# Performance work log

Measured on AMD Instinct MI355X. Metric: run time of the kernel, lower is better.

The kernel has to match this reference:

```python
import jax, jax.numpy as jnp
import numpy as np

B, N_REG, D_IN = 32, 116, 256
N_NODES = B * N_REG            # 3712
E_PER_G = N_REG * 10           # avg degree 10
E = B * E_PER_G                # 37120
HEADS = 8
HID = [256, 128, 64]
D_OUT = 256
LN_EPS = 1e-5


def _layer_norm(x, scale, bias):
    mu = x.mean(-1, keepdims=True)
    var = ((x - mu) ** 2).mean(-1, keepdims=True)
    return (x - mu) * jax.lax.rsqrt(var + LN_EPS) * scale + bias


def _gat_layer(x, W, b, a_src, a_dst, src, dst, concat):
    """PyG-style GATConv (shared lin, self-loops, leaky_relu 0.2) + ELU + LayerNorm."""
    N = x.shape[0]
    H, C = a_src.shape
    h = (x @ W).reshape(N, H, C)                      # (N, H, C)
    sl = jnp.arange(N, dtype=src.dtype)               # self-loops (PyG default)
    s = jnp.concatenate([src, sl])
    d = jnp.concatenate([dst, sl])
    al = (h * a_src).sum(-1)                          # (N, H)
    ar = (h * a_dst).sum(-1)                          # (N, H)
    e = jax.nn.leaky_relu(al[s] + ar[d], 0.2)         # (E', H)
    m = jax.ops.segment_max(e, d, num_segments=N)
    ex = jnp.exp(e - m[d])
    den = jax.ops.segment_sum(ex, d, num_segments=N)
    alpha = ex / den[d]                               # segment softmax over incoming edges
    out = jax.ops.segment_sum(h[s] * alpha[..., None], d, num_segments=N)  # (N, H, C)
    out = out.reshape(N, H * C) if concat else out.mean(1)
    return out + b


def setup_inputs() -> dict:
    key = jax.random.key(0)
    ks = list(jax.random.split(key, 32))
    node_features = jax.random.normal(ks[0], (N_NODES, D_IN), dtype=jnp.float32)
    # edges: random within each graph (disconnected batched graph)
    off = (jnp.arange(B, dtype=jnp.int32) * N_REG)[:, None]
    src = (jax.random.randint(ks[1], (B, E_PER_G), 0, N_REG, dtype=jnp.int32) + off).reshape(-1)
    dst = (jax.random.randint(ks[2], (B, E_PER_G), 0, N_REG, dtype=jnp.int32) + off).reshape(-1)
    batch = jnp.repeat(jnp.arange(B, dtype=jnp.int32), N_REG)

    def lin(k, fin, fout):
        s = 1.0 / np.sqrt(fin)
        return jax.random.uniform(k, (fin, fout), jnp.float32, -s, s)

    dims_in = [D_IN, HID[0] * HEADS, HID[1] * HEADS]
    p = {}
    ki = 3
    for i, (fin, c) in enumerate(zip(dims_in, HID)):
        concat = i < len(HID) - 1
        wdim = c * HEADS
        p[f"w{i}"] = lin(ks[ki], fin, wdim); ki += 1
        p[f"b{i}"] = jnp.zeros((wdim if concat else c,), jnp.float32)
        p[f"as{i}"] = jax.random.normal(ks[ki], (HEADS, c), jnp.float32) * 0.1; ki += 1
        p[f"ad{i}"] = jax.random.normal(ks[ki], (HEADS, c), jnp.float32) * 0.1; ki += 1
        ldim = wdim if concat else c
        p[f"ls{i}"] = jnp.ones((ldim,), jnp.float32)
        p[f"lb{i}"] = jnp.zeros((ldim,), jnp.float32)
    p["wp"] = lin(ks[ki], HID[-1], D_OUT); ki += 1
    p["bp"] = jnp.zeros((D_OUT,), jnp.float32)
    p["lsp"] = jnp.ones((D_OUT,), jnp.float32)
    p["lbp"] = jnp.zeros((D_OUT,), jnp.float32)
    p["wq"] = lin(ks[ki], D_OUT, 1); ki += 1
    p["bq"] = jnp.zeros((1,), jnp.float32)
    return dict(node_features=node_features, src=src, dst=dst, batch=batch, **p)


def reference(node_features, src, dst, batch,
              w0, b0, as0, ad0, ls0, lb0,
              w1, b1, as1, ad1, ls1, lb1,
              w2, b2, as2, ad2, ls2, lb2,
              wp, bp, lsp, lbp, wq, bq):
    x = node_features
    x = _layer_norm(jax.nn.elu(_gat_layer(x, w0, b0, as0, ad0, src, dst, True)), ls0, lb0)
    x = _layer_norm(jax.nn.elu(_gat_layer(x, w1, b1, as1, ad1, src, dst, True)), ls1, lb1)
    x = _layer_norm(jax.nn.elu(_gat_layer(x, w2, b2, as2, ad2, src, dst, False)), ls2, lb2)
    node_out = jax.nn.gelu(_layer_norm(x @ wp + bp, lsp, lbp), approximate=False)  # (N, 256)
    pool_w = jax.nn.softmax(node_out @ wq + bq, axis=0)                            # (N, 1) global softmax
    num = jax.ops.segment_sum(node_out * pool_w, batch, num_segments=B)            # (B, 256)
    den = jnp.maximum(jax.ops.segment_sum(pool_w, batch, num_segments=B), 1e-8)    # (B, 1)
    graph_features = num / den
    return graph_features, node_out
```

## Files before the change

### kernel.cpp

```cpp
#include <hip/hip_runtime.h>
#include <hip/hip_bf16.h>
#include <math.h>

typedef __hip_bfloat16 bf16;
typedef short short8 __attribute__((ext_vector_type(8)));
typedef float f32x4 __attribute__((ext_vector_type(4)));

__device__ __forceinline__ float b2f(const bf16 v) { return __bfloat162float(v); }
__device__ __forceinline__ bf16 f2b(const float v) { return __float2bfloat16(v); }

__device__ __forceinline__ float bits2f(short s) {
  unsigned u = ((unsigned)(unsigned short)s) << 16;
  float f;
  __builtin_memcpy(&f, &u, 4);
  return f;
}
__device__ __forceinline__ short f2bits(float f) {
  bf16 b = f2b(f);
  short s;
  __builtin_memcpy(&s, &b, 2);
  return s;
}

__device__ __forceinline__ float ldsel(const void* p, size_t i, int f32) {
  return f32 ? ((const float*)p)[i] : b2f(((const bf16*)p)[i]);
}
__device__ __forceinline__ void stsel(void* p, size_t i, float v, int f32) {
  if (f32) ((float*)p)[i] = v; else ((bf16*)p)[i] = f2b(v);
}

#define NN 3712
#define NE 37120
#define NG 32
#define NREG 116
#define MAXDEG 48

__global__ __launch_bounds__(256) void k_detect(const void* nf, const void* w0, int* flags) {
  __shared__ int bad[2];
  if (threadIdx.x < 2) bad[threadIdx.x] = 0;
  __syncthreads();
  const bf16* a = (const bf16*)nf;
  const bf16* b = (const bf16*)w0;
  int l0 = 0, l1 = 0;
  for (int i = threadIdx.x; i < 4096; i += 256) {
    float x = b2f(a[i]); if (!(fabsf(x) < 1e4f)) l0++;
    float y = b2f(b[i]); if (!(fabsf(y) < 1e4f)) l1++;
  }
  if (l0) atomicAdd(&bad[0], l0);
  if (l1) atomicAdd(&bad[1], l1);
  __syncthreads();
  if (threadIdx.x == 0) { flags[0] = bad[0] > 0; flags[1] = bad[1] > 0; }
}

__global__ __launch_bounds__(256) void k_zero(int* __restrict__ p, int n) {
  int i = blockIdx.x * 256 + threadIdx.x;
  if (i < n) p[i] = 0;
}

__global__ __launch_bounds__(256) void k_scatter(const int* __restrict__ src, const int* __restrict__ dst,
                                                 int* __restrict__ cnt, int* __restrict__ bucket, int E) {
  int e = blockIdx.x * 256 + threadIdx.x;
  if (e < E) {
    int d = dst[e], s = src[e];
    if ((unsigned)d < NN && (unsigned)s < NN) {
      int p = atomicAdd(&cnt[d], 1);
      if (p < MAXDEG) bucket[d * MAXDEG + p] = s;
    }
  }
}

__global__ __launch_bounds__(256) void k_tobf16(const void* __restrict__ in, bf16* __restrict__ out,
                                                int n, const int* __restrict__ flags, int fidx) {
  int f = flags[fidx];
  int i = blockIdx.x * 256 + threadIdx.x;
  if (i < n) out[i] = f2b(ldsel(in, i, f));
}

__global__ __launch_bounds__(256) void k_transpose(const void* __restrict__ W, bf16* __restrict__ Wt,
                                                   int K, int N, const int* __restrict__ flags) {
  int f = flags[1];
  __shared__ float tile[32][33];
  int tx = threadIdx.x & 31, ty = threadIdx.x >> 5;
  int k0 = blockIdx.x * 32, n0 = blockIdx.y * 32;
#pragma unroll
  for (int i = 0; i < 4; ++i)
    tile[ty + i * 8][tx] = ldsel(W, (size_t)(k0 + ty + i * 8) * N + n0 + tx, f);
  __syncthreads();
#pragma unroll
  for (int i = 0; i < 4; ++i)
    Wt[(size_t)(n0 + ty + i * 8) * K + k0 + tx] = f2b(tile[tx][ty + i * 8]);
}

__global__ __launch_bounds__(256) void k_gemm_mfma(const bf16* __restrict__ A, const bf16* __restrict__ Bt,
                                                   bf16* __restrict__ C, int M, int N, int K) {
  __shared__ short As[64 * 72];
  __shared__ short Bs[64 * 72];
  int tid = threadIdx.x;
  int wave = tid >> 6, lane = tid & 63;
  int wr = wave >> 1, wc = wave & 1;
  int quad = lane >> 4, ml = lane & 15;

  int nbx = N >> 6;
  int total = gridDim.x;
  int id = blockIdx.x;
  int tile = ((total & 7) == 0) ? ((id & 7) * (total >> 3) + (id >> 3)) : id;
  int n0 = (tile % nbx) << 6;
  int m0 = (tile / nbx) << 6;

  f32x4 acc[2][2];
#pragma unroll
  for (int rt = 0; rt < 2; ++rt)
#pragma unroll
    for (int ct = 0; ct < 2; ++ct)
#pragma unroll
      for (int r = 0; r < 4; ++r) acc[rt][ct][r] = 0.f;

  for (int k0 = 0; k0 < K; k0 += 64) {
    __syncthreads();
#pragma unroll
    for (int i = 0; i < 2; ++i) {
      int c = tid + (i << 8);
      int row = c >> 3, kg = (c & 7) << 3;
      *(uint4*)&As[row * 72 + kg] = *(const uint4*)&A[(size_t)(m0 + row) * K + k0 + kg];
      *(uint4*)&Bs[row * 72 + kg] = *(const uint4*)&Bt[(size_t)(n0 + row) * K + k0 + kg];
    }
    __syncthreads();
    short8 af[2][2], bfr[2][2];
#pragma unroll
    for (int rt = 0; rt < 2; ++rt)
#pragma unroll
      for (int kk = 0; kk < 2; ++kk)
        af[rt][kk] = *(const short8*)&As[(wr * 32 + rt * 16 + ml) * 72 + kk * 32 + quad * 8];
#pragma unroll
    for (int ct = 0; ct < 2; ++ct)
#pragma unroll
      for (int kk = 0; kk < 2; ++kk)
        bfr[ct][kk] = *(const short8*)&Bs[(wc * 32 + ct * 16 + ml) * 72 + kk * 32 + quad * 8];
#pragma unroll
    for (int rt = 0; rt < 2; ++rt)
#pragma unroll
      for (int ct = 0; ct < 2; ++ct)
#pragma unroll
        for (int kk = 0; kk < 2; ++kk)
          acc[rt][ct] = __builtin_amdgcn_mfma_f32_16x16x32_bf16(af[rt][kk], bfr[ct][kk], acc[rt][ct], 0, 0, 0);
  }
#pragma unroll
  for (int rt = 0; rt < 2; ++rt)
#pragma unroll
    for (int ct = 0; ct < 2; ++ct)
#pragma unroll
      for (int r = 0; r < 4; ++r) {
        int grow = m0 + wr * 32 + rt * 16 + quad * 4 + r;
        int gcol = n0 + wc * 32 + ct * 16 + ml;
        C[(size_t)grow * N + gcol] = f2b(acc[rt][ct][r]);
      }
}

__global__ void k_attn(const bf16* __restrict__ H, const void* __restrict__ a_s,
                       const void* __restrict__ a_d, float* __restrict__ al,
                       float* __restrict__ ar, int C, const int* __restrict__ flags) {
  int wF = flags[1];
  int t = threadIdx.x;
  int D = 8 * C;
  int i0 = t * 8;
  float as8[8], ad8[8];
#pragma unroll
  for (int j = 0; j < 8; ++j) { as8[j] = ldsel(a_s, i0 + j, wF); ad8[j] = ldsel(a_d, i0 + j, wF); }
  int G = C >> 3;
  int hd = i0 / C;
  for (int it = 0; it < 8; ++it) {
    int n = blockIdx.x * 8 + it;
    union { short8 v; short s[8]; } u;
    u.v = *(const short8*)&H[(size_t)n * D + i0];
    float ps = 0.f, pd = 0.f;
#pragma unroll
    for (int j = 0; j < 8; ++j) {
      float h = bits2f(u.s[j]);
      ps = fmaf(h, as8[j], ps);
      pd = fmaf(h, ad8[j], pd);
    }
    for (int off = G >> 1; off; off >>= 1) {
      ps += __shfl_xor(ps, off);
      pd += __shfl_xor(pd, off);
    }
    if ((t & (G - 1)) == 0) {
      al[n * 8 + hd] = ps;
      ar[n * 8 + hd] = pd;
    }
  }
}

__global__ __launch_bounds__(256) void k_edgew(const float* __restrict__ al, const float* __restrict__ ar,
                                               const int* __restrict__ cnt, const int* __restrict__ bucket,
                                               float* __restrict__ mbuf, float* __restrict__ ibuf) {
  int t = threadIdx.x;
  int q = t >> 6, l = t & 63, hd = l >> 3, el = l & 7;
  int d = blockIdx.x * 4 + q;
  int deg = cnt[d]; deg = deg > MAXDEG ? MAXDEG : deg;
  int total = deg + 1;
  float ard = ar[d * 8 + hd];
  float lgv[7];
  float m = -1e30f;
#pragma unroll
  for (int k = 0; k < 7; ++k) {
    int e = el + k * 8;
    float lg = -1e30f;
    if (e < total) {
      int s = e < deg ? bucket[d * MAXDEG + e] : d;
      lg = al[s * 8 + hd] + ard;
      lg = lg > 0.f ? lg : 0.2f * lg;
    }
    lgv[k] = lg;
    m = fmaxf(m, lg);
  }
#pragma unroll
  for (int off = 4; off; off >>= 1) m = fmaxf(m, __shfl_xor(m, off));
  float den = 0.f;
#pragma unroll
  for (int k = 0; k < 7; ++k) den += (lgv[k] > -1e29f) ? expf(lgv[k] - m) : 0.f;
#pragma unroll
  for (int off = 4; off; off >>= 1) den += __shfl_xor(den, off);
  if (el == 0) { mbuf[d * 8 + hd] = m; ibuf[d * 8 + hd] = 1.f / den; }
}

__global__ void k_agg(const bf16* __restrict__ H, const float* __restrict__ al,
                      const float* __restrict__ ar, const float* __restrict__ mbuf,
                      const float* __restrict__ ibuf, const int* __restrict__ cnt,
                      const int* __restrict__ bucket, const void* __restrict__ bias,
                      const void* __restrict__ ls, const void* __restrict__ lb,
                      bf16* __restrict__ Xout, int C, int concat,
                      const int* __restrict__ flags) {
  int wF = flags[1];
  int bid = blockIdx.x;
  int x = bid & 7, jj = bid >> 3;
  int d = (x + ((jj / NREG) << 3)) * NREG + (jj % NREG);
  int t = threadIdx.x;
  int nt = blockDim.x;
  int lane = t & 63, wave = t >> 6;
  int D = 8 * C;
  __shared__ int sid[MAXDEG + 4];
  __shared__ float vals[512];
  __shared__ float r1[4], r2[4];
  __shared__ float sMu, sRs;

  int deg = cnt[d]; deg = deg > MAXDEG ? MAXDEG : deg;
  int total = deg + 1;
  int padded = (total + 3) & ~3;
  if (t < padded) sid[t] = t < deg ? bucket[d * MAXDEG + t] : d;
  __syncthreads();

  int i0 = t * 8;
  int hd = i0 / C;
  float m = mbuf[d * 8 + hd], inv = ibuf[d * 8 + hd], ard = ar[d * 8 + hd];

  float acc[8] = {0.f, 0.f, 0.f, 0.f, 0.f, 0.f, 0.f, 0.f};
  const bf16* __restrict__ Hp = H + i0;
  for (int eb = 0; eb < padded; eb += 4) {
    int s4[4]; float a4[4]; short8 u4[4];
#pragma unroll
    for (int j = 0; j < 4; ++j) s4[j] = sid[eb + j];
#pragma unroll
    for (int j = 0; j < 4; ++j) {
      a4[j] = al[s4[j] * 8 + hd];
      u4[j] = *(const short8*)&Hp[(size_t)s4[j] * D];
    }
#pragma unroll
    for (int j = 0; j < 4; ++j) {
      float lg = a4[j] + ard;
      lg = lg > 0.f ? lg : 0.2f * lg;
      float we = (eb + j) < total ? expf(lg - m) * inv : 0.f;
      union { short8 v; short s[8]; } uu; uu.v = u4[j];
#pragma unroll
      for (int k2 = 0; k2 < 8; ++k2) acc[k2] = fmaf(we, bits2f(uu.s[k2]), acc[k2]);
    }
  }

  if (concat) {
    float v[8];
    float s1 = 0.f, s2 = 0.f;
#pragma unroll
    for (int j = 0; j < 8; ++j) {
      float vv = acc[j] + ldsel(bias, i0 + j, wF);
      vv = vv > 0.f ? vv : expf(vv) - 1.f;
      v[j] = vv; s1 += vv; s2 += vv * vv;
    }
#pragma unroll
    for (int off = 32; off; off >>= 1) { s1 += __shfl_down(s1, off); s2 += __shfl_down(s2, off); }
    if (lane == 0) { r1[wave] = s1; r2[wave] = s2; }
    __syncthreads();
    if (t == 0) {
      float S1 = 0.f, S2 = 0.f;
      int nw = nt >> 6;
      for (int i = 0; i < nw; ++i) { S1 += r1[i]; S2 += r2[i]; }
      float mu = S1 / D;
      sMu = mu; sRs = rsqrtf(S2 / D - mu * mu + 1e-5f);
    }
    __syncthreads();
    union { short8 v; short s[8]; } ou;
#pragma unroll
    for (int j = 0; j < 8; ++j)
      ou.s[j] = f2bits((v[j] - sMu) * sRs * ldsel(ls, i0 + j, wF) + ldsel(lb, i0 + j, wF));
    *(short8*)&Xout[(size_t)d * D + i0] = ou.v;
  } else {
#pragma unroll
    for (int j = 0; j < 8; ++j) vals[i0 + j] = acc[j];
    __syncthreads();
    float v = 0.f;
#pragma unroll
    for (int h = 0; h < 8; ++h) v += vals[h * 64 + t];
    v = v * 0.125f + ldsel(bias, t, wF);
    v = v > 0.f ? v : expf(v) - 1.f;
    float s1 = v, s2 = v * v;
#pragma unroll
    for (int off = 32; off; off >>= 1) { s1 += __shfl_xor(s1, off); s2 += __shfl_xor(s2, off); }
    float mu = s1 * (1.f / 64.f);
    float var = s2 * (1.f / 64.f) - mu * mu;
    float rs = rsqrtf(var + 1e-5f);
    Xout[(size_t)d * 64 + t] = f2b((v - mu) * rs * ldsel(ls, t, wF) + ldsel(lb, t, wF));
  }
}

__global__ __launch_bounds__(256) void k_proj(const bf16* __restrict__ X3, const void* __restrict__ wp,
                                              const void* __restrict__ bp, const void* __restrict__ lsp,
                                              const void* __restrict__ lbp, const void* __restrict__ wq,
                                              const void* __restrict__ bq,
                                              float* __restrict__ q, void* __restrict__ dout,
                                              const int* __restrict__ flags) {
  int wF = flags[1], xF = flags[0];
  int n = blockIdx.x, t = threadIdx.x;
  int lane = t & 63, wave = t >> 6;
  __shared__ float xs[64];
  __shared__ float r1[4], r2[4];
  __shared__ float sMu, sRs;
  if (t < 64) xs[t] = b2f(X3[n * 64 + t]);
  __syncthreads();
  float y = ldsel(bp, t, wF);
#pragma unroll 8
  for (int k = 0; k < 64; ++k) y = fmaf(xs[k], ldsel(wp, k * 256 + t, wF), y);
  float s1 = y, s2 = y * y;
#pragma unroll
  for (int off = 32; off; off >>= 1) { s1 += __shfl_down(s1, off); s2 += __shfl_down(s2, off); }
  if (lane == 0) { r1[wave] = s1; r2[wave] = s2; }
  __syncthreads();
  if (t == 0) {
    float S1 = r1[0] + r1[1] + r1[2] + r1[3];
    float S2 = r2[0] + r2[1] + r2[2] + r2[3];
    float mu = S1 / 256.f;
    sMu = mu; sRs = rsqrtf(S2 / 256.f - mu * mu + 1e-5f);
  }
  __syncthreads();
  float v = (y - sMu) * sRs * ldsel(lsp, t, wF) + ldsel(lbp, t, wF);
  float g = 0.5f * v * (1.f + erff(v * 0.70710678118654752f));
  stsel(dout, (size_t)NG * 256 + (size_t)n * 256 + t, g, xF);
  float qv = g * ldsel(wq, t, wF);
#pragma unroll
  for (int off = 32; off; off >>= 1) qv += __shfl_down(qv, off);
  if (lane == 0) r1[wave] = qv;
  __syncthreads();
  if (t == 0) q[n] = r1[0] + r1[1] + r1[2] + r1[3] + ldsel(bq, 0, wF);
}

__global__ __launch_bounds__(256) void k_pool(void* __restrict__ dout, const float* __restrict__ q,
                                              const int* __restrict__ flags) {
  int xF = flags[0];
  int b = blockIdx.x, t = threadIdx.x;
  __shared__ float es[NREG];
  __shared__ float sDen;
  if (t < NREG) es[t] = q[b * NREG + t];
  __syncthreads();
  if (t == 0) {
    float m = -1e30f;
    for (int i = 0; i < NREG; ++i) m = fmaxf(m, es[i]);
    float den = 0.f;
    for (int i = 0; i < NREG; ++i) { float e = expf(es[i] - m); es[i] = e; den += e; }
    sDen = den;
  }
  __syncthreads();
  float acc = 0.f;
  for (int i = 0; i < NREG; ++i)
    acc = fmaf(es[i], ldsel(dout, (size_t)NG * 256 + (size_t)(b * NREG + i) * 256 + t, xF), acc);
  stsel(dout, (size_t)b * 256 + t, acc / sDen, xF);
}

extern "C" void kernel_launch(void* const* d_in, const int* in_sizes, int n_in,
                              void* d_out, int out_size, void* d_ws, size_t ws_size,
                              hipStream_t stream) {
  const void* nf  = d_in[0];
  const int* src  = (const int*)d_in[1];
  const int* dst  = (const int*)d_in[2];
  const void *w0 = d_in[4],  *b0 = d_in[5],  *as0 = d_in[6], *ad0 = d_in[7],  *ls0 = d_in[8],  *lb0 = d_in[9];
  const void *w1 = d_in[10], *b1 = d_in[11], *as1 = d_in[12], *ad1 = d_in[13], *ls1 = d_in[14], *lb1 = d_in[15];
  const void *w2 = d_in[16], *b2 = d_in[17], *as2 = d_in[18], *ad2 = d_in[19], *ls2 = d_in[20], *lb2 = d_in[21];
  const void *wp = d_in[22], *bp = d_in[23], *lsp = d_in[24], *lbp = d_in[25], *wq = d_in[26], *bq = d_in[27];

  int* flags  = (int*)d_ws;
  float* al   = (float*)(flags + 4);
  float* ar   = al + NN * 8;
  int* cnt    = (int*)(ar + NN * 8);
  int* bucket = cnt + NN;
  float* q    = (float*)(bucket + NN * MAXDEG);
  bf16* X     = (bf16*)(q + NN);
  bf16* Hb    = X + (size_t)NN * 2048;

  float* mbuf = (float*)d_out;
  float* ibuf = mbuf + NN * 8;

  bf16* X0  = X;
  bf16* wt0 = X + (1 << 20);
  bf16* wt1 = Hb + (size_t)NN * 1024;
  bf16* wt2 = Hb + (size_t)NN * 512;

  k_detect<<<1, 256, 0, stream>>>(nf, w0, flags);
  k_zero<<<(NN + 255) / 256, 256, 0, stream>>>(cnt, NN);
  k_scatter<<<(NE + 255) / 256, 256, 0, stream>>>(src, dst, cnt, bucket, NE);
  k_tobf16<<<(NN * 256 + 255) / 256, 256, 0, stream>>>(nf, X0, NN * 256, flags, 0);

  k_transpose<<<dim3(256 / 32, 2048 / 32), 256, 0, stream>>>(w0, wt0, 256, 2048, flags);
  k_gemm_mfma<<<(2048 / 64) * (NN / 64), 256, 0, stream>>>(X0, wt0, Hb, NN, 2048, 256);
  k_attn<<<NN / 8, 256, 0, stream>>>(Hb, as0, ad0, al, ar, 256, flags);
  k_edgew<<<NN / 4, 256, 0, stream>>>(al, ar, cnt, bucket, mbuf, ibuf);
  k_agg<<<NN, 256, 0, stream>>>(Hb, al, ar, mbuf, ibuf, cnt, bucket, b0, ls0, lb0, X, 256, 1, flags);

  k_transpose<<<dim3(2048 / 32, 1024 / 32), 256, 0, stream>>>(w1, wt1, 2048, 1024, flags);
  k_gemm_mfma<<<(1024 / 64) * (NN / 64), 256, 0, stream>>>(X, wt1, Hb, NN, 1024, 2048);
  k_attn<<<NN / 8, 128, 0, stream>>>(Hb, as1, ad1, al, ar, 128, flags);
  k_edgew<<<NN / 4, 256, 0, stream>>>(al, ar, cnt, bucket, mbuf, ibuf);
  k_agg<<<NN, 128, 0, stream>>>(Hb, al, ar, mbuf, ibuf, cnt, bucket, b1, ls1, lb1, X, 128, 1, flags);

  k_transpose<<<dim3(1024 / 32, 512 / 32), 256, 0, stream>>>(w2, wt2, 1024, 512, flags);
  k_gemm_mfma<<<(512 / 64) * (NN / 64), 256, 0, stream>>>(X, wt2, Hb, NN, 512, 1024);
  k_attn<<<NN / 8, 64, 0, stream>>>(Hb, as2, ad2, al, ar, 64, flags);
  k_edgew<<<NN / 4, 256, 0, stream>>>(al, ar, cnt, bucket, mbuf, ibuf);
  k_agg<<<NN, 64, 0, stream>>>(Hb, al, ar, mbuf, ibuf, cnt, bucket, b2, ls2, lb2, X, 64, 0, flags);

  k_proj<<<NN, 256, 0, stream>>>(X, wp, bp, lsp, lbp, wq, bq, q, d_out, flags);
  k_pool<<<NG, 256, 0, stream>>>(d_out, q, flags);
}
```

Measured before the change: 366.8 us.

## Replace per-node gather aggregation with per-graph dense MFMA attention matmul

For the two concat GAT layers, edge aggregation now builds a dense 116x116 bf16 attention matrix per (graph, head) in shared memory and multiplies it with the transposed head features using MFMA instructions. This replaces the per-node gather of neighbour rows. Bias, ELU and LayerNorm move into a separate k_ln kernel. The intent is to turn irregular gathers into dense tensor-core work that reuses H within each graph. The trade-offs are an extra pass over X, only 256 blocks with large LDS use, and duplicate-edge weights summed in bf16 precision.

```diff
diff --git a/kernel.cpp b/kernel.cpp
--- a/kernel.cpp
+++ b/kernel.cpp
@@ -221,6 +221,143 @@
 #pragma unroll
   for (int off = 4; off; off >>= 1) den += __shfl_xor(den, off);
   if (el == 0) { mbuf[d * 8 + hd] = m; ibuf[d * 8 + hd] = 1.f / den; }
+}
+
+template<int C>
+__global__ __launch_bounds__(256, 1) void k_aggm(const bf16* __restrict__ H,
+    const float* __restrict__ al, const float* __restrict__ ar,
+    const float* __restrict__ mbuf, const float* __restrict__ ibuf,
+    const int* __restrict__ cnt, const int* __restrict__ bucket,
+    bf16* __restrict__ Y) {
+  constexpr int D = 8 * C;
+  constexpr int KP = 136;
+  __shared__ short P[128 * KP];
+  __shared__ short Ht[C * KP];
+  int t = threadIdx.x;
+  int bid = blockIdx.x;
+  int h = bid >> 5, g = bid & 31;
+  int gbase = g * NREG;
+
+  short8 z = {0, 0, 0, 0, 0, 0, 0, 0};
+  for (int i = t; i < 128 * KP / 8; i += 256) *(short8*)&P[i * 8] = z;
+  for (int i = t; i < C * KP / 8; i += 256) *(short8*)&Ht[i * 8] = z;
+  __syncthreads();
+
+  constexpr int CH = C / 8;
+  for (int idx = t; idx < NREG * CH; idx += 256) {
+    int s = idx / CH, c0 = (idx % CH) * 8;
+    union { short8 v; short x[8]; } u;
+    u.v = *(const short8*)&H[(size_t)(gbase + s) * D + h * C + c0];
+#pragma unroll
+    for (int j = 0; j < 8; ++j) Ht[(c0 + j) * KP + s] = u.x[j];
+  }
+  if (t < NREG) {
+    int gd = gbase + t;
+    int deg = cnt[gd]; deg = deg > MAXDEG ? MAXDEG : deg;
+    int total = deg + 1;
+    float ard = ar[gd * 8 + h];
+    float mm = mbuf[gd * 8 + h], inv = ibuf[gd * 8 + h];
+    for (int base = 0; base < total; base += 8) {
+      int sg[8]; float av[8];
+#pragma unroll
+      for (int j = 0; j < 8; ++j) {
+        int e = base + j;
+        sg[j] = (e < deg) ? bucket[gd * MAXDEG + e] : gd;
+      }
+#pragma unroll
+      for (int j = 0; j < 8; ++j) av[j] = al[sg[j] * 8 + h];
+#pragma unroll
+      for (int j = 0; j < 8; ++j) {
+        if (base + j < total) {
+          float lg = av[j] + ard;
+          lg = lg > 0.f ? lg : 0.2f * lg;
+          float alpha = expf(lg - mm) * inv;
+          int off = t * KP + (sg[j] - gbase);
+          P[off] = f2bits(bits2f(P[off]) + alpha);
+        }
+      }
+    }
+  }
+  __syncthreads();
+
+  constexpr int CT = C / 32;
+  int wave = t >> 6, lane = t & 63;
+  int wr = wave >> 1, wc = wave & 1;
+  int quad = lane >> 4, ml = lane & 15;
+  f32x4 acc[4][CT];
+#pragma unroll
+  for (int a = 0; a < 4; ++a)
+#pragma unroll
+    for (int b = 0; b < CT; ++b)
+#pragma unroll
+      for (int r = 0; r < 4; ++r) acc[a][b][r] = 0.f;
+#pragma unroll
+  for (int ks = 0; ks < 4; ++ks) {
+    short8 af[4], bf8[CT];
+#pragma unroll
+    for (int rt = 0; rt < 4; ++rt)
+      af[rt] = *(const short8*)&P[(wr * 64 + rt * 16 + ml) * KP + ks * 32 + quad * 8];
+#pragma unroll
+    for (int ct = 0; ct < CT; ++ct)
+      bf8[ct] = *(const short8*)&Ht[(wc * (C / 2) + ct * 16 + ml) * KP + ks * 32 + quad * 8];
+#pragma unroll
+    for (int rt = 0; rt < 4; ++rt)
+#pragma unroll
+      for (int ct = 0; ct < CT; ++ct)
+        acc[rt][ct] = __builtin_amdgcn_mfma_f32_16x16x32_bf16(af[rt], bf8[ct], acc[rt][ct], 0, 0, 0);
+  }
+#pragma unroll
+  for (int rt = 0; rt < 4; ++rt) {
+    int m = wr * 64 + rt * 16 + quad * 4;
+#pragma unroll
+    for (int r = 0; r < 4; ++r) {
+      if (m + r < NREG) {
+#pragma unroll
+        for (int ct = 0; ct < CT; ++ct) {
+          int n = wc * (C / 2) + ct * 16 + ml;
+          Y[(size_t)(gbase + m + r) * D + h * C + n] = f2b(acc[rt][ct][r]);
+        }
+      }
+    }
+  }
+}
+
+template<int D>
+__global__ __launch_bounds__(256) void k_ln(bf16* __restrict__ X, const void* __restrict__ bias,
+                                            const void* __restrict__ ls, const void* __restrict__ lb,
+                                            const int* __restrict__ flags) {
+  int wF = flags[1];
+  constexpr int VPT = D / 256;
+  int t = threadIdx.x;
+  int node = blockIdx.x * 8 + (t >> 5);
+  int l32 = t & 31;
+  float v[VPT * 8];
+  float s1 = 0.f, s2 = 0.f;
+#pragma unroll
+  for (int j = 0; j < VPT; ++j) {
+    int c0 = (l32 + j * 32) * 8;
+    union { short8 u; short x[8]; } uu;
+    uu.u = *(const short8*)&X[(size_t)node * D + c0];
+#pragma unroll
+    for (int k = 0; k < 8; ++k) {
+      float vv = bits2f(uu.x[k]) + ldsel(bias, c0 + k, wF);
+      vv = vv > 0.f ? vv : expf(vv) - 1.f;
+      v[j * 8 + k] = vv; s1 += vv; s2 += vv * vv;
+    }
+  }
+#pragma unroll
+  for (int off = 16; off; off >>= 1) { s1 += __shfl_xor(s1, off); s2 += __shfl_xor(s2, off); }
+  float mu = s1 / D;
+  float rs = rsqrtf(s2 / D - mu * mu + 1e-5f);
+#pragma unroll
+  for (int j = 0; j < VPT; ++j) {
+    int c0 = (l32 + j * 32) * 8;
+    union { short8 u; short x[8]; } uu;
+#pragma unroll
+    for (int k = 0; k < 8; ++k)
+      uu.x[k] = f2bits((v[j * 8 + k] - mu) * rs * ldsel(ls, c0 + k, wF) + ldsel(lb, c0 + k, wF));
+    *(short8*)&X[(size_t)node * D + c0] = uu.u;
+  }
 }
 
 __global__ void k_agg(const bf16* __restrict__ H, const float* __restrict__ al,
@@ -235,13 +372,9 @@
   int x = bid & 7, jj = bid >> 3;
   int d = (x + ((jj / NREG) << 3)) * NREG + (jj % NREG);
   int t = threadIdx.x;
-  int nt = blockDim.x;
-  int lane = t & 63, wave = t >> 6;
   int D = 8 * C;
   __shared__ int sid[MAXDEG + 4];
   __shared__ float vals[512];
-  __shared__ float r1[4], r2[4];
-  __shared__ float sMu, sRs;
 
   int deg = cnt[d]; deg = deg > MAXDEG ? MAXDEG : deg;
   int total = deg + 1;
@@ -275,49 +408,21 @@
     }
   }
 
-  if (concat) {
-    float v[8];
-    float s1 = 0.f, s2 = 0.f;
-#pragma unroll
-    for (int j = 0; j < 8; ++j) {
-      float vv = acc[j] + ldsel(bias, i0 + j, wF);
-      vv = vv > 0.f ? vv : expf(vv) - 1.f;
-      v[j] = vv; s1 += vv; s2 += vv * vv;
-    }
-#pragma unroll
-    for (int off = 32; off; off >>= 1) { s1 += __shfl_down(s1, off); s2 += __shfl_down(s2, off); }
-    if (lane == 0) { r1[wave] = s1; r2[wave] = s2; }
-    __syncthreads();
-    if (t == 0) {
-      float S1 = 0.f, S2 = 0.f;
-      int nw = nt >> 6;
-      for (int i = 0; i < nw; ++i) { S1 += r1[i]; S2 += r2[i]; }
-      float mu = S1 / D;
-      sMu = mu; sRs = rsqrtf(S2 / D - mu * mu + 1e-5f);
-    }
-    __syncthreads();
-    union { short8 v; short s[8]; } ou;
-#pragma unroll
-    for (int j = 0; j < 8; ++j)
-      ou.s[j] = f2bits((v[j] - sMu) * sRs * ldsel(ls, i0 + j, wF) + ldsel(lb, i0 + j, wF));
-    *(short8*)&Xout[(size_t)d * D + i0] = ou.v;
-  } else {
-#pragma unroll
-    for (int j = 0; j < 8; ++j) vals[i0 + j] = acc[j];
-    __syncthreads();
-    float v = 0.f;
-#pragma unroll
-    for (int h = 0; h < 8; ++h) v += vals[h * 64 + t];
-    v = v * 0.125f + ldsel(bias, t, wF);
-    v = v > 0.f ? v : expf(v) - 1.f;
-    float s1 = v, s2 = v * v;
-#pragma unroll
-    for (int off = 32; off; off >>= 1) { s1 += __shfl_xor(s1, off); s2 += __shfl_xor(s2, off); }
-    float mu = s1 * (1.f / 64.f);
-    float var = s2 * (1.f / 64.f) - mu * mu;
-    float rs = rsqrtf(var + 1e-5f);
-    Xout[(size_t)d * 64 + t] = f2b((v - mu) * rs * ldsel(ls, t, wF) + ldsel(lb, t, wF));
-  }
+#pragma unroll
+  for (int j = 0; j < 8; ++j) vals[i0 + j] = acc[j];
+  __syncthreads();
+  float v = 0.f;
+#pragma unroll
+  for (int h = 0; h < 8; ++h) v += vals[h * 64 + t];
+  v = v * 0.125f + ldsel(bias, t, wF);
+  v = v > 0.f ? v : expf(v) - 1.f;
+  float s1 = v, s2 = v * v;
+#pragma unroll
+  for (int off = 32; off; off >>= 1) { s1 += __shfl_xor(s1, off); s2 += __shfl_xor(s2, off); }
+  float mu = s1 * (1.f / 64.f);
+  float var = s2 * (1.f / 64.f) - mu * mu;
+  float rs = rsqrtf(var + 1e-5f);
+  Xout[(size_t)d * 64 + t] = f2b((v - mu) * rs * ldsel(ls, t, wF) + ldsel(lb, t, wF));
 }
 
 __global__ __launch_bounds__(256) void k_proj(const bf16* __restrict__ X3, const void* __restrict__ wp,
@@ -419,13 +524,15 @@
   k_gemm_mfma<<<(2048 / 64) * (NN / 64), 256, 0, stream>>>(X0, wt0, Hb, NN, 2048, 256);
   k_attn<<<NN / 8, 256, 0, stream>>>(Hb, as0, ad0, al, ar, 256, flags);
   k_edgew<<<NN / 4, 256, 0, stream>>>(al, ar, cnt, bucket, mbuf, ibuf);
-  k_agg<<<NN, 256, 0, stream>>>(Hb, al, ar, mbuf, ibuf, cnt, bucket, b0, ls0, lb0, X, 256, 1, flags);
+  k_aggm<256><<<256, 256, 0, stream>>>(Hb, al, ar, mbuf, ibuf, cnt, bucket, X);
+  k_ln<2048><<<NN / 8, 256, 0, stream>>>(X, b0, ls0, lb0, flags);
 
   k_transpose<<<dim3(2048 / 32, 1024 / 32), 256, 0, stream>>>(w1, wt1, 2048, 1024, flags);
   k_gemm_mfma<<<(1024 / 64) * (NN / 64), 256, 0, stream>>>(X, wt1, Hb, NN, 1024, 2048);
   k_attn<<<NN / 8, 128, 0, stream>>>(Hb, as1, ad1, al, ar, 128, flags);
   k_edgew<<<NN / 4, 256, 0, stream>>>(al, ar, cnt, bucket, mbuf, ibuf);
-  k_agg<<<NN, 128, 0, stream>>>(Hb, al, ar, mbuf, ibuf, cnt, bucket, b1, ls1, lb1, X, 128, 1, flags);
+  k_aggm<128><<<256, 256, 0, stream>>>(Hb, al, ar, mbuf, ibuf, cnt, bucket, X);
+  k_ln<1024><<<NN / 8, 256, 0, stream>>>(X, b1, ls1, lb1, flags);
 
   k_transpose<<<dim3(1024 / 32, 512 / 32), 256, 0, stream>>>(w2, wt2, 1024, 512, flags);
   k_gemm_mfma<<<(512 / 64) * (NN / 64), 256, 0, stream>>>(X, wt2, Hb, NN, 512, 1024);
```

New measurement: 392.6 us. 7.0% more time.
